# Kernel optimization log

Measured on AMD Instinct MI355X. Metric: run time of the kernel, lower is better.

Reference implementation:

```python
import jax, jax.numpy as jnp
import numpy as np

N_NODES = 20000
N_EDGES = 320000
NUM_GRAPHS = 64
IN_DIM = 256


def setup_inputs() -> dict:
    key = jax.random.key(0)
    ks = jax.random.split(key, 12)
    x = jax.random.normal(ks[0], (N_NODES, IN_DIM), dtype=jnp.float32)
    edge_index = jax.random.randint(ks[1], (2, N_EDGES), 0, N_NODES, dtype=jnp.int64)
    batch = jnp.sort(jax.random.randint(ks[2], (N_NODES,), 0, NUM_GRAPHS, dtype=jnp.int64))
    def glorot(k, shape):
        lim = float(np.sqrt(6.0 / (shape[0] + shape[1])))
        return jax.random.uniform(k, shape, dtype=jnp.float32, minval=-lim, maxval=lim)
    W1 = glorot(ks[3], (IN_DIM, 256)); b1 = jnp.zeros((256,), jnp.float32)
    W2 = glorot(ks[4], (256, 128));   b2 = jnp.zeros((128,), jnp.float32)
    Wl1 = glorot(ks[5], (128, 64));   bl1 = jnp.zeros((64,), jnp.float32)
    Wl2 = glorot(ks[6], (64, 1));     bl2 = jnp.zeros((1,), jnp.float32)
    return {"x": x, "edge_index": edge_index, "batch": batch,
            "W1": W1, "b1": b1, "W2": W2, "b2": b2,
            "Wl1": Wl1, "bl1": bl1, "Wl2": Wl2, "bl2": bl2}


def gcn_conv(x, src, dst, W, b, n_nodes):
    # PyG GCNConv: add self-loops, symmetric normalization D^-1/2 (A+I) D^-1/2,
    # linear transform first, then gather-scale-scatter aggregation, then bias.
    loop = jnp.arange(n_nodes, dtype=src.dtype)
    s = jnp.concatenate([src, loop])
    d = jnp.concatenate([dst, loop])
    deg = jax.ops.segment_sum(jnp.ones_like(d, dtype=x.dtype), d, num_segments=n_nodes)
    dinv = jnp.where(deg > 0, jax.lax.rsqrt(deg), 0.0)
    norm = dinv[s] * dinv[d]                         # [E+N]
    h = x @ W                                        # [N, out]
    msg = h[s] * norm[:, None]                       # [E+N, out]
    out = jax.ops.segment_sum(msg, d, num_segments=n_nodes)
    return out + b


def global_mean_pool(x, batch, num_graphs):
    sums = jax.ops.segment_sum(x, batch, num_segments=num_graphs)
    cnts = jax.ops.segment_sum(jnp.ones((x.shape[0],), x.dtype), batch, num_segments=num_graphs)
    return sums / jnp.maximum(cnts, 1.0)[:, None]


def reference(x, edge_index, batch, W1, b1, W2, b2, Wl1, bl1, Wl2, bl2):
    n = x.shape[0]
    src, dst = edge_index[0], edge_index[1]
    h = jax.nn.relu(gcn_conv(x, src, dst, W1, b1, n))   # dropout = identity (eval)
    h = jax.nn.relu(gcn_conv(h, src, dst, W2, b2, n))
    g = global_mean_pool(h, batch, NUM_GRAPHS)          # [G, 128]
    g = jax.nn.relu(g @ Wl1 + bl1)
    return jax.nn.sigmoid(g @ Wl2 + bl2)                # [G, 1]
```

## Files before the change

### kernel.cpp

```cpp
#include <hip/hip_runtime.h>
#include <hip/hip_bf16.h>
#include <math.h>

typedef __attribute__((ext_vector_type(8))) short bf16x8;
typedef __attribute__((ext_vector_type(4))) float f32x4;

__device__ __forceinline__ unsigned short f2bf(float f) {
    unsigned int u = __float_as_uint(f);
    unsigned int r = (u + 0x7FFFu + ((u >> 16) & 1u)) >> 16;
    return (unsigned short)r;
}
__device__ __forceinline__ unsigned int pk2bf(float lo, float hi) {
    unsigned int r;
    asm("v_cvt_pk_bf16_f32 %0, %1, %2" : "=v"(r) : "v"(lo), "v"(hi));
    return r;
}
__device__ __forceinline__ unsigned char f2fp8(float v) {
    int p = __builtin_amdgcn_cvt_pk_fp8_f32(v, v, 0, false);
    return (unsigned char)(p & 0xff);
}
__device__ __forceinline__ unsigned int pk4fp8(float a, float b, float c, float d) {
    int p = __builtin_amdgcn_cvt_pk_fp8_f32(a, b, 0, false);
    p = __builtin_amdgcn_cvt_pk_fp8_f32(c, d, p, true);
    return (unsigned int)p;
}
__device__ __forceinline__ void fp8x8_fma(uint2 u, float w, float* a) {
    a[0] += __builtin_amdgcn_cvt_f32_fp8((int)u.x, 0) * w;
    a[1] += __builtin_amdgcn_cvt_f32_fp8((int)u.x, 1) * w;
    a[2] += __builtin_amdgcn_cvt_f32_fp8((int)u.x, 2) * w;
    a[3] += __builtin_amdgcn_cvt_f32_fp8((int)u.x, 3) * w;
    a[4] += __builtin_amdgcn_cvt_f32_fp8((int)u.y, 0) * w;
    a[5] += __builtin_amdgcn_cvt_f32_fp8((int)u.y, 1) * w;
    a[6] += __builtin_amdgcn_cvt_f32_fp8((int)u.y, 2) * w;
    a[7] += __builtin_amdgcn_cvt_f32_fp8((int)u.y, 3) * w;
}
__device__ __forceinline__ void fp8x4_fma(unsigned int u, float w, float* a) {
    a[0] += __builtin_amdgcn_cvt_f32_fp8((int)u, 0) * w;
    a[1] += __builtin_amdgcn_cvt_f32_fp8((int)u, 1) * w;
    a[2] += __builtin_amdgcn_cvt_f32_fp8((int)u, 2) * w;
    a[3] += __builtin_amdgcn_cvt_f32_fp8((int)u, 3) * w;
}
__device__ __forceinline__ float deg_dinv(int c) { return rsqrtf((float)c + 1.0f); }

__device__ __forceinline__ void load_lds16(const unsigned short* g, unsigned short* l) {
    __builtin_amdgcn_global_load_lds(
        (const __attribute__((address_space(1))) unsigned int*)g,
        (__attribute__((address_space(3))) unsigned int*)l, 16, 0, 0);
}
__device__ __forceinline__ void load_lds16_u8(const unsigned char* g, unsigned char* l) {
    __builtin_amdgcn_global_load_lds(
        (const __attribute__((address_space(1))) unsigned int*)g,
        (__attribute__((address_space(3))) unsigned int*)l, 16, 0, 0);
}

__global__ __launch_bounds__(256) void prep_kernel(const int* __restrict__ batch,
                                                   int* __restrict__ gstart,
                                                   const float* __restrict__ W1,
                                                   unsigned short* __restrict__ w1t,
                                                   const float* __restrict__ W2,
                                                   unsigned char* __restrict__ w2t8,
                                                   int N, int G, int BNB) {
    int b = blockIdx.x;
    int tid = threadIdx.x;
    if (b < BNB) {
        int i = b * 256 + tid;
        if (i >= N) return;
        int bb = batch[i];
        if (i == 0) { for (int g = 0; g <= bb; g++) gstart[g] = 0; }
        else { int bp = batch[i - 1]; for (int g = bp + 1; g <= bb; g++) gstart[g] = i; }
        if (i == N - 1) { for (int g = bb + 1; g <= G; g++) gstart[g] = N; }
        return;
    }
    int idx = (b - BNB) * 256 + tid;
    if (idx < 256 * 256) {
        int m = idx >> 8, k = idx & 255;
        w1t[idx] = f2bf(W1[(size_t)k * 256 + m]);
    } else if (idx < 256 * 256 + 128 * 256) {
        int j = idx - 256 * 256;
        int m = j >> 8, k = j & 255;
        w2t8[j] = f2fp8(W2[(size_t)k * 128 + m]);
    }
}

__global__ __launch_bounds__(256) void fill_gemm1_kernel(const int* __restrict__ src,
                                                         const int* __restrict__ dst,
                                                         int* __restrict__ cnt,
                                                         int* __restrict__ csr,
                                                         const float* __restrict__ x,
                                                         const unsigned short* __restrict__ Bt,
                                                         unsigned char* __restrict__ C8,
                                                         int N, int E, int FB) {
    __shared__ unsigned short As[128 * 32];
    __shared__ unsigned short Bs[128 * 32];
    if ((int)blockIdx.x < FB) {
        int e = (blockIdx.x * 256 + threadIdx.x) * 4;
        if (e + 3 < E) {
            int4 d4 = *(const int4*)(dst + e);
            int4 s4 = *(const int4*)(src + e);
            int sl;
            sl = atomicAdd(&cnt[d4.x], 1); if (sl < 64) csr[(d4.x << 6) + sl] = s4.x;
            sl = atomicAdd(&cnt[d4.y], 1); if (sl < 64) csr[(d4.y << 6) + sl] = s4.y;
            sl = atomicAdd(&cnt[d4.z], 1); if (sl < 64) csr[(d4.z << 6) + sl] = s4.z;
            sl = atomicAdd(&cnt[d4.w], 1); if (sl < 64) csr[(d4.w << 6) + sl] = s4.w;
        } else {
            for (; e < E; e++) {
                int d = dst[e];
                int slot = atomicAdd(&cnt[d], 1);
                if (slot < 64) csr[(d << 6) + slot] = src[e];
            }
        }
        return;
    }
    int gb = blockIdx.x - FB;
    int bx = gb & 1, by = gb >> 1;
    const int K = 256;
    int tid = threadIdx.x;
    int wave = tid >> 6, lane = tid & 63;
    int quad = lane >> 4, m16 = lane & 15;
    int r0 = by * 128, c0 = bx * 128;
    int srow = lane >> 2;
    int skoff = (lane & 3) * 8;

    f32x4 acc[2][8];
#pragma unroll
    for (int rg = 0; rg < 2; rg++)
#pragma unroll
        for (int ct = 0; ct < 8; ct++) acc[rg][ct] = (f32x4){0.f, 0.f, 0.f, 0.f};

    int arow = tid >> 1, akh = tid & 1;
    int agrow = r0 + arow; if (agrow >= N) agrow = N - 1;
    const float* ap = x + (size_t)agrow * K + akh * 16;
    int asw = (arow >> 1) & 3;
    unsigned short* as0 = As + arow * 32 + ((((akh << 1) | 0) ^ asw) << 3);
    unsigned short* as1 = As + arow * 32 + ((((akh << 1) | 1) ^ asw) << 3);
    int rsw = (m16 >> 1) & 3;

    for (int kb = 0; kb < K; kb += 32) {
        float4 f0 = *(const float4*)(ap + kb);
        float4 f1 = *(const float4*)(ap + kb + 4);
        float4 f2 = *(const float4*)(ap + kb + 8);
        float4 f3 = *(const float4*)(ap + kb + 12);
        {
            int bcol = wave * 16 + srow;
            load_lds16(Bt + (size_t)(c0 + bcol) * K + kb + skoff, Bs + (wave * 16) * 32);
            load_lds16(Bt + (size_t)(c0 + 64 + bcol) * K + kb + skoff, Bs + (64 + wave * 16) * 32);
        }
        uint4 u0, u1;
        u0.x = pk2bf(f0.x, f0.y); u0.y = pk2bf(f0.z, f0.w);
        u0.z = pk2bf(f1.x, f1.y); u0.w = pk2bf(f1.z, f1.w);
        u1.x = pk2bf(f2.x, f2.y); u1.y = pk2bf(f2.z, f2.w);
        u1.z = pk2bf(f3.x, f3.y); u1.w = pk2bf(f3.z, f3.w);
        *(uint4*)as0 = u0;
        *(uint4*)as1 = u1;
        __syncthreads();
        bf16x8 af[2], bfr[8];
#pragma unroll
        for (int rg = 0; rg < 2; rg++)
            af[rg] = *(const bf16x8*)(As + (wave * 32 + rg * 16 + m16) * 32 + ((quad ^ rsw) << 3));
#pragma unroll
        for (int ct = 0; ct < 8; ct++)
            bfr[ct] = *(const bf16x8*)(Bs + (ct * 16 + m16) * 32 + (quad << 3));
#pragma unroll
        for (int rg = 0; rg < 2; rg++)
#pragma unroll
            for (int ct = 0; ct < 8; ct++)
                acc[rg][ct] = __builtin_amdgcn_mfma_f32_16x16x32_bf16(af[rg], bfr[ct], acc[rg][ct], 0, 0, 0);
        __syncthreads();
    }
#pragma unroll
    for (int rg = 0; rg < 2; rg++) {
#pragma unroll
        for (int ct = 0; ct < 8; ct++) {
            int col = c0 + ct * 16 + m16;
#pragma unroll
            for (int r = 0; r < 4; r++) {
                int row = r0 + wave * 32 + rg * 16 + quad * 4 + r;
                if (row < N) C8[(size_t)row * 256 + col] = f2fp8(acc[rg][ct][r]);
            }
        }
    }
}

__global__ __launch_bounds__(256) void gemm2_kernel(const unsigned char* __restrict__ A,
                                                    const unsigned char* __restrict__ Bt,
                                                    unsigned char* __restrict__ C8, int N) {
    __shared__ unsigned char As8[128 * 32];
    __shared__ unsigned char Bs8[64 * 32];
    const int K = 256;
    int tid = threadIdx.x;
    int wave = tid >> 6, lane = tid & 63;
    int quad = lane >> 4, m16 = lane & 15;
    int bx = blockIdx.x, by = blockIdx.y;
    int r0 = by * 128, c0 = bx * 64;

    f32x4 acc[2][4];
#pragma unroll
    for (int rg = 0; rg < 2; rg++)
#pragma unroll
        for (int ct = 0; ct < 4; ct++) acc[rg][ct] = (f32x4){0.f, 0.f, 0.f, 0.f};

    int arow = wave * 32 + (lane >> 1);
    int agrow = r0 + arow; if (agrow >= N) agrow = N - 1;
    int ach = (lane & 1) * 16;
    int brow = (wave & 1) * 32 + (lane >> 1);
    int bch = (lane & 1) * 16;

    for (int kb = 0; kb < K; kb += 32) {
        load_lds16_u8(A + (size_t)agrow * K + kb + ach, As8 + (wave * 32) * 32);
        if (wave < 2)
            load_lds16_u8(Bt + (size_t)(c0 + brow) * K + kb + bch, Bs8 + (wave * 32) * 32);
        __syncthreads();
        long af[2], bfr[4];
#pragma unroll
        for (int rg = 0; rg < 2; rg++)
            af[rg] = *(const long*)(As8 + (wave * 32 + rg * 16 + m16) * 32 + (quad << 3));
#pragma unroll
        for (int ct = 0; ct < 4; ct++)
            bfr[ct] = *(const long*)(Bs8 + (ct * 16 + m16) * 32 + (quad << 3));
#pragma unroll
        for (int rg = 0; rg < 2; rg++)
#pragma unroll
            for (int ct = 0; ct < 4; ct++)
                acc[rg][ct] = __builtin_amdgcn_mfma_f32_16x16x32_fp8_fp8(af[rg], bfr[ct], acc[rg][ct], 0, 0, 0);
        __syncthreads();
    }
#pragma unroll
    for (int rg = 0; rg < 2; rg++) {
#pragma unroll
        for (int ct = 0; ct < 4; ct++) {
            int col = c0 + ct * 16 + m16;
#pragma unroll
            for (int r = 0; r < 4; r++) {
                int row = r0 + wave * 32 + rg * 16 + quad * 4 + r;
                if (row < N) C8[(size_t)row * 128 + col] = f2fp8(acc[rg][ct][r]);
            }
        }
    }
}

__global__ __launch_bounds__(256) void gather256_kernel(const unsigned char* __restrict__ h8,
                                                        const int* __restrict__ csr,
                                                        const int* __restrict__ cnt,
                                                        const float* __restrict__ bias,
                                                        unsigned char* __restrict__ o18, int N) {
    int node = blockIdx.x * 4 + (threadIdx.x >> 6);
    if (node >= N) return;
    int lane = threadIdx.x & 63;
    int half = lane >> 5, hl = lane & 31;
    int beg = node << 6;
    int c = cnt[node]; if (c > 64) c = 64;
    int end = beg + c;
    float a[8] = {0, 0, 0, 0, 0, 0, 0, 0};
    int j = beg;
    for (; j + 7 < end; j += 8) {
        int s0 = csr[j + half], s1 = csr[j + 2 + half];
        int s2 = csr[j + 4 + half], s3 = csr[j + 6 + half];
        float w0 = deg_dinv(cnt[s0]), w1 = deg_dinv(cnt[s1]);
        float w2 = deg_dinv(cnt[s2]), w3 = deg_dinv(cnt[s3]);
        uint2 u0 = *(const uint2*)(h8 + (size_t)s0 * 256 + hl * 8);
        uint2 u1 = *(const uint2*)(h8 + (size_t)s1 * 256 + hl * 8);
        uint2 u2 = *(const uint2*)(h8 + (size_t)s2 * 256 + hl * 8);
        uint2 u3 = *(const uint2*)(h8 + (size_t)s3 * 256 + hl * 8);
        fp8x8_fma(u0, w0, a); fp8x8_fma(u1, w1, a);
        fp8x8_fma(u2, w2, a); fp8x8_fma(u3, w3, a);
    }
    for (; j + 1 < end; j += 2) {
        int s0 = csr[j + half];
        float w0 = deg_dinv(cnt[s0]);
        uint2 u0 = *(const uint2*)(h8 + (size_t)s0 * 256 + hl * 8);
        fp8x8_fma(u0, w0, a);
    }
    if (j < end && half == 0) {
        int s0 = csr[j];
        float w0 = deg_dinv(cnt[s0]);
        uint2 u0 = *(const uint2*)(h8 + (size_t)s0 * 256 + hl * 8);
        fp8x8_fma(u0, w0, a);
    }
#pragma unroll
    for (int i = 0; i < 8; i++) a[i] += __shfl_down(a[i], 32);
    if (half == 0) {
        float dd = deg_dinv(c);
        float self[8] = {0, 0, 0, 0, 0, 0, 0, 0};
        uint2 uh = *(const uint2*)(h8 + (size_t)node * 256 + hl * 8);
        fp8x8_fma(uh, dd, self);
        float4 bv0 = ((const float4*)bias)[hl * 2];
        float4 bv1 = ((const float4*)bias)[hl * 2 + 1];
        float bvf[8] = {bv0.x, bv0.y, bv0.z, bv0.w, bv1.x, bv1.y, bv1.z, bv1.w};
        float v[8];
#pragma unroll
        for (int i = 0; i < 8; i++) v[i] = fmaxf((a[i] + self[i]) * dd + bvf[i], 0.f);
        uint2 o;
        o.x = pk4fp8(v[0], v[1], v[2], v[3]);
        o.y = pk4fp8(v[4], v[5], v[6], v[7]);
        ((uint2*)(o18 + (size_t)node * 256))[hl] = o;
    }
}

__global__ __launch_bounds__(256) void gather128_kernel(const unsigned char* __restrict__ t8,
                                                        const int* __restrict__ csr,
                                                        const int* __restrict__ cnt,
                                                        const float* __restrict__ bias,
                                                        unsigned char* __restrict__ out2, int N) {
    int node = blockIdx.x * 4 + (threadIdx.x >> 6);
    if (node >= N) return;
    int lane = threadIdx.x & 63;
    int half = lane >> 5, hl = lane & 31;
    int beg = node << 6;
    int c = cnt[node]; if (c > 64) c = 64;
    int end = beg + c;
    float a[4] = {0, 0, 0, 0};
    int j = beg;
    for (; j + 7 < end; j += 8) {
        int s0 = csr[j + half], s1 = csr[j + 2 + half];
        int s2 = csr[j + 4 + half], s3 = csr[j + 6 + half];
        float w0 = deg_dinv(cnt[s0]), w1 = deg_dinv(cnt[s1]);
        float w2 = deg_dinv(cnt[s2]), w3 = deg_dinv(cnt[s3]);
        unsigned int u0 = *(const unsigned int*)(t8 + (size_t)s0 * 128 + hl * 4);
        unsigned int u1 = *(const unsigned int*)(t8 + (size_t)s1 * 128 + hl * 4);
        unsigned int u2 = *(const unsigned int*)(t8 + (size_t)s2 * 128 + hl * 4);
        unsigned int u3 = *(const unsigned int*)(t8 + (size_t)s3 * 128 + hl * 4);
        fp8x4_fma(u0, w0, a); fp8x4_fma(u1, w1, a);
        fp8x4_fma(u2, w2, a); fp8x4_fma(u3, w3, a);
    }
    for (; j + 1 < end; j += 2) {
        int s0 = csr[j + half];
        float w0 = deg_dinv(cnt[s0]);
        unsigned int u0 = *(const unsigned int*)(t8 + (size_t)s0 * 128 + hl * 4);
        fp8x4_fma(u0, w0, a);
    }
    if (j < end && half == 0) {
        int s0 = csr[j];
        float w0 = deg_dinv(cnt[s0]);
        unsigned int u0 = *(const unsigned int*)(t8 + (size_t)s0 * 128 + hl * 4);
        fp8x4_fma(u0, w0, a);
    }
#pragma unroll
    for (int i = 0; i < 4; i++) a[i] += __shfl_down(a[i], 32);
    if (half == 0) {
        float dd = deg_dinv(c);
        float self[4] = {0, 0, 0, 0};
        unsigned int uh = *(const unsigned int*)(t8 + (size_t)node * 128 + hl * 4);
        fp8x4_fma(uh, dd, self);
        float4 bv = ((const float4*)bias)[hl];
        float r0 = fmaxf((a[0] + self[0]) * dd + bv.x, 0.f);
        float r1 = fmaxf((a[1] + self[1]) * dd + bv.y, 0.f);
        float r2 = fmaxf((a[2] + self[2]) * dd + bv.z, 0.f);
        float r3 = fmaxf((a[3] + self[3]) * dd + bv.w, 0.f);
        ((unsigned int*)(out2 + (size_t)node * 128))[hl] = pk4fp8(r0, r1, r2, r3);
    }
}

__global__ __launch_bounds__(256) void poolhead_kernel(const unsigned char* __restrict__ out2,
                                                       const int* __restrict__ gstart,
                                                       float* __restrict__ gsum,
                                                       int* __restrict__ gdone,
                                                       const float* __restrict__ Wl1,
                                                       const float* __restrict__ bl1,
                                                       const float* __restrict__ Wl2,
                                                       const float* __restrict__ bl2,
                                                       float* __restrict__ out) {
    int g = blockIdx.x >> 3, slice = blockIdx.x & 7;
    int tid = threadIdx.x;
    int hw = tid >> 5, hl = tid & 31;
    int gs = gstart[g], ge = gstart[g + 1];
    float a[4] = {0, 0, 0, 0};
    for (int i = gs + slice * 8 + hw; i < ge; i += 64) {
        unsigned int u = ((const unsigned int*)(out2 + (size_t)i * 128))[hl];
        fp8x4_fma(u, 1.0f, a);
    }
    __shared__ float red[8][128];
#pragma unroll
    for (int k = 0; k < 4; k++) red[hw][hl * 4 + k] = a[k];
    __syncthreads();
    if (tid < 128) {
        float s = 0.f;
#pragma unroll
        for (int w = 0; w < 8; w++) s += red[w][tid];
        if (s != 0.f) atomicAdd(&gsum[g * 128 + tid], s);
    }
    __syncthreads();
    __shared__ int lastflag;
    if (tid == 0) {
        __threadfence();
        int old = atomicAdd(&gdone[g], 1);
        lastflag = (old == 7) ? 1 : 0;
    }
    __syncthreads();
    if (!lastflag) return;
    __shared__ float gv[128];
    if (tid < 128) {
        float s = atomicAdd(&gsum[g * 128 + tid], 0.0f);
        float cntf = fmaxf((float)(ge - gs), 1.0f);
        gv[tid] = s / cntf;
    }
    __syncthreads();
    if (tid < 64) {
        float acc = bl1[tid];
#pragma unroll 8
        for (int k = 0; k < 128; k++) acc += gv[k] * Wl1[k * 64 + tid];
        acc = fmaxf(acc, 0.f);
        float p = acc * Wl2[tid];
#pragma unroll
        for (int off = 32; off; off >>= 1) p += __shfl_down(p, off);
        if (tid == 0) out[g] = 1.f / (1.f + expf(-(p + bl2[0])));
    }
}

extern "C" void kernel_launch(void* const* d_in, const int* in_sizes, int n_in,
                              void* d_out, int out_size, void* d_ws, size_t ws_size,
                              hipStream_t stream) {
    const float* x   = (const float*)d_in[0];
    const int* ei    = (const int*)d_in[1];
    const int* batch = (const int*)d_in[2];
    const float* W1  = (const float*)d_in[3];
    const float* b1  = (const float*)d_in[4];
    const float* W2  = (const float*)d_in[5];
    const float* b2  = (const float*)d_in[6];
    const float* Wl1 = (const float*)d_in[7];
    const float* bl1 = (const float*)d_in[8];
    const float* Wl2 = (const float*)d_in[9];
    const float* bl2 = (const float*)d_in[10];
    float* out = (float*)d_out;

    const int N = in_sizes[2];
    const int E = in_sizes[1] / 2;
    const int G = 64;
    const int* src = ei;
    const int* dst = ei + E;

    char* base = (char*)d_ws;
    size_t off = 0;
    auto carve = [&](size_t bytes) -> char* {
        char* p = base + off;
        off = (off + bytes + 15) & ~(size_t)15;
        return p;
    };
    int*   cnt    = (int*)carve((size_t)N * 4);
    float* gsum   = (float*)carve((size_t)G * 128 * 4);
    int*   gdone  = (int*)carve((size_t)G * 4);
    size_t zero_bytes = (size_t)(N + G * 128 + G) * 4 + 32;
    int*   csr    = (int*)carve((size_t)N * 64 * 4);
    int*   gstart = (int*)carve((size_t)(G + 1) * 4);
    unsigned short* w1t  = (unsigned short*)carve((size_t)256 * 256 * 2);
    unsigned char*  w2t8 = (unsigned char*)carve((size_t)128 * 256);
    unsigned char*  h8   = (unsigned char*)carve((size_t)N * 256);
    unsigned char*  o18  = (unsigned char*)carve((size_t)N * 256);
    unsigned char*  t8   = h8;
    unsigned char*  out2 = o18;

    hipMemsetAsync(d_ws, 0, zero_bytes, stream);

    const int BNB = (N + 255) / 256;
    const int CWB = (256 * 256 + 128 * 256 + 255) / 256;
    prep_kernel<<<BNB + CWB, 256, 0, stream>>>(batch, gstart, W1, w1t, W2, w2t8, N, G, BNB);

    const int FB  = (E / 4 + 255) / 256;
    const int GB1 = 2 * ((N + 127) / 128);
    fill_gemm1_kernel<<<FB + GB1, 256, 0, stream>>>(src, dst, cnt, csr,
                                                    x, w1t, h8, N, E, FB);

    gather256_kernel<<<(N + 3) / 4, 256, 0, stream>>>(h8, csr, cnt, b1, o18, N);

    {
        dim3 grid(2, (N + 127) / 128);
        gemm2_kernel<<<grid, 256, 0, stream>>>(o18, w2t8, t8, N);
    }
    gather128_kernel<<<(N + 3) / 4, 256, 0, stream>>>(t8, csr, cnt, b2, out2, N);

    poolhead_kernel<<<G * 8, 256, 0, stream>>>(out2, gstart, gsum, gdone,
                                               Wl1, bl1, Wl2, bl2, out);
}
```

Baseline: 171.2 us.

## Fold source-degree normalization into GEMM epilogues and reorganize kernel fusion

Premultiplies each GEMM output row by its dinv so the gather kernels no longer load cnt[src] and compute rsqrt per edge; gathers become plain fp8 sums. Edge CSR fill is moved into the prep kernel so GEMM1 can read final degrees, which costs fusing fill with GEMM1 concurrency. Gather loops are unrolled to 16 neighbours and use packed fp8->f32 conversion when available. Pre-scaling before fp8 quantization slightly changes rounding behaviour.

After: 173.1 us. Within noise of the previous version (+1.1%).

```diff
diff --git a/kernel.cpp b/kernel.cpp
--- a/kernel.cpp
+++ b/kernel.cpp
@@ -4,6 +4,7 @@
 
 typedef __attribute__((ext_vector_type(8))) short bf16x8;
 typedef __attribute__((ext_vector_type(4))) float f32x4;
+typedef __attribute__((ext_vector_type(2))) float f32x2;
 
 __device__ __forceinline__ unsigned short f2bf(float f) {
     unsigned int u = __float_as_uint(f);
@@ -24,22 +25,38 @@
     p = __builtin_amdgcn_cvt_pk_fp8_f32(c, d, p, true);
     return (unsigned int)p;
 }
-__device__ __forceinline__ void fp8x8_fma(uint2 u, float w, float* a) {
-    a[0] += __builtin_amdgcn_cvt_f32_fp8((int)u.x, 0) * w;
-    a[1] += __builtin_amdgcn_cvt_f32_fp8((int)u.x, 1) * w;
-    a[2] += __builtin_amdgcn_cvt_f32_fp8((int)u.x, 2) * w;
-    a[3] += __builtin_amdgcn_cvt_f32_fp8((int)u.x, 3) * w;
-    a[4] += __builtin_amdgcn_cvt_f32_fp8((int)u.y, 0) * w;
-    a[5] += __builtin_amdgcn_cvt_f32_fp8((int)u.y, 1) * w;
-    a[6] += __builtin_amdgcn_cvt_f32_fp8((int)u.y, 2) * w;
-    a[7] += __builtin_amdgcn_cvt_f32_fp8((int)u.y, 3) * w;
-}
-__device__ __forceinline__ void fp8x4_fma(unsigned int u, float w, float* a) {
-    a[0] += __builtin_amdgcn_cvt_f32_fp8((int)u, 0) * w;
-    a[1] += __builtin_amdgcn_cvt_f32_fp8((int)u, 1) * w;
-    a[2] += __builtin_amdgcn_cvt_f32_fp8((int)u, 2) * w;
-    a[3] += __builtin_amdgcn_cvt_f32_fp8((int)u, 3) * w;
-}
+#if __has_builtin(__builtin_amdgcn_cvt_pk_f32_fp8)
+__device__ __forceinline__ void fp8x8_add(uint2 u, float* a) {
+    f32x2 p0 = __builtin_amdgcn_cvt_pk_f32_fp8((int)u.x, false);
+    f32x2 p1 = __builtin_amdgcn_cvt_pk_f32_fp8((int)u.x, true);
+    f32x2 p2 = __builtin_amdgcn_cvt_pk_f32_fp8((int)u.y, false);
+    f32x2 p3 = __builtin_amdgcn_cvt_pk_f32_fp8((int)u.y, true);
+    a[0] += p0.x; a[1] += p0.y; a[2] += p1.x; a[3] += p1.y;
+    a[4] += p2.x; a[5] += p2.y; a[6] += p3.x; a[7] += p3.y;
+}
+__device__ __forceinline__ void fp8x4_add(unsigned int u, float* a) {
+    f32x2 p0 = __builtin_amdgcn_cvt_pk_f32_fp8((int)u, false);
+    f32x2 p1 = __builtin_amdgcn_cvt_pk_f32_fp8((int)u, true);
+    a[0] += p0.x; a[1] += p0.y; a[2] += p1.x; a[3] += p1.y;
+}
+#else
+__device__ __forceinline__ void fp8x8_add(uint2 u, float* a) {
+    a[0] += __builtin_amdgcn_cvt_f32_fp8((int)u.x, 0);
+    a[1] += __builtin_amdgcn_cvt_f32_fp8((int)u.x, 1);
+    a[2] += __builtin_amdgcn_cvt_f32_fp8((int)u.x, 2);
+    a[3] += __builtin_amdgcn_cvt_f32_fp8((int)u.x, 3);
+    a[4] += __builtin_amdgcn_cvt_f32_fp8((int)u.y, 0);
+    a[5] += __builtin_amdgcn_cvt_f32_fp8((int)u.y, 1);
+    a[6] += __builtin_amdgcn_cvt_f32_fp8((int)u.y, 2);
+    a[7] += __builtin_amdgcn_cvt_f32_fp8((int)u.y, 3);
+}
+__device__ __forceinline__ void fp8x4_add(unsigned int u, float* a) {
+    a[0] += __builtin_amdgcn_cvt_f32_fp8((int)u, 0);
+    a[1] += __builtin_amdgcn_cvt_f32_fp8((int)u, 1);
+    a[2] += __builtin_amdgcn_cvt_f32_fp8((int)u, 2);
+    a[3] += __builtin_amdgcn_cvt_f32_fp8((int)u, 3);
+}
+#endif
 __device__ __forceinline__ float deg_dinv(int c) { return rsqrtf((float)c + 1.0f); }
 
 __device__ __forceinline__ void load_lds16(const unsigned short* g, unsigned short* l) {
@@ -53,47 +70,21 @@
         (__attribute__((address_space(3))) unsigned int*)l, 16, 0, 0);
 }
 
-__global__ __launch_bounds__(256) void prep_kernel(const int* __restrict__ batch,
-                                                   int* __restrict__ gstart,
-                                                   const float* __restrict__ W1,
-                                                   unsigned short* __restrict__ w1t,
-                                                   const float* __restrict__ W2,
-                                                   unsigned char* __restrict__ w2t8,
-                                                   int N, int G, int BNB) {
+__global__ __launch_bounds__(256) void prepfill_kernel(const int* __restrict__ src,
+                                                       const int* __restrict__ dst,
+                                                       int* __restrict__ cnt,
+                                                       int* __restrict__ csr,
+                                                       const int* __restrict__ batch,
+                                                       int* __restrict__ gstart,
+                                                       const float* __restrict__ W1,
+                                                       unsigned short* __restrict__ w1t,
+                                                       const float* __restrict__ W2,
+                                                       unsigned char* __restrict__ w2t8,
+                                                       int N, int G, int E, int FB, int CWB) {
     int b = blockIdx.x;
     int tid = threadIdx.x;
-    if (b < BNB) {
-        int i = b * 256 + tid;
-        if (i >= N) return;
-        int bb = batch[i];
-        if (i == 0) { for (int g = 0; g <= bb; g++) gstart[g] = 0; }
-        else { int bp = batch[i - 1]; for (int g = bp + 1; g <= bb; g++) gstart[g] = i; }
-        if (i == N - 1) { for (int g = bb + 1; g <= G; g++) gstart[g] = N; }
-        return;
-    }
-    int idx = (b - BNB) * 256 + tid;
-    if (idx < 256 * 256) {
-        int m = idx >> 8, k = idx & 255;
-        w1t[idx] = f2bf(W1[(size_t)k * 256 + m]);
-    } else if (idx < 256 * 256 + 128 * 256) {
-        int j = idx - 256 * 256;
-        int m = j >> 8, k = j & 255;
-        w2t8[j] = f2fp8(W2[(size_t)k * 128 + m]);
-    }
-}
-
-__global__ __launch_bounds__(256) void fill_gemm1_kernel(const int* __restrict__ src,
-                                                         const int* __restrict__ dst,
-                                                         int* __restrict__ cnt,
-                                                         int* __restrict__ csr,
-                                                         const float* __restrict__ x,
-                                                         const unsigned short* __restrict__ Bt,
-                                                         unsigned char* __restrict__ C8,
-                                                         int N, int E, int FB) {
-    __shared__ unsigned short As[128 * 32];
-    __shared__ unsigned short Bs[128 * 32];
-    if ((int)blockIdx.x < FB) {
-        int e = (blockIdx.x * 256 + threadIdx.x) * 4;
+    if (b < FB) {
+        int e = (b * 256 + tid) * 4;
         if (e + 3 < E) {
             int4 d4 = *(const int4*)(dst + e);
             int4 s4 = *(const int4*)(src + e);
@@ -111,7 +102,37 @@
         }
         return;
     }
-    int gb = blockIdx.x - FB;
+    b -= FB;
+    if (b < CWB) {
+        int idx = b * 256 + tid;
+        if (idx < 256 * 256) {
+            int m = idx >> 8, k = idx & 255;
+            w1t[idx] = f2bf(W1[(size_t)k * 256 + m]);
+        } else if (idx < 256 * 256 + 128 * 256) {
+            int j = idx - 256 * 256;
+            int m = j >> 8, k = j & 255;
+            w2t8[j] = f2fp8(W2[(size_t)k * 128 + m]);
+        }
+        return;
+    }
+    b -= CWB;
+    {
+        int i = b * 256 + tid;
+        if (i >= N) return;
+        int bb = batch[i];
+        if (i == 0) { for (int g = 0; g <= bb; g++) gstart[g] = 0; }
+        else { int bp = batch[i - 1]; for (int g = bp + 1; g <= bb; g++) gstart[g] = i; }
+        if (i == N - 1) { for (int g = bb + 1; g <= G; g++) gstart[g] = N; }
+    }
+}
+
+__global__ __launch_bounds__(256) void gemm1_kernel(const float* __restrict__ x,
+                                                    const unsigned short* __restrict__ Bt,
+                                                    const int* __restrict__ cnt,
+                                                    unsigned char* __restrict__ C8, int N) {
+    __shared__ unsigned short As[128 * 32];
+    __shared__ unsigned short Bs[128 * 32];
+    int gb = blockIdx.x;
     int bx = gb & 1, by = gb >> 1;
     const int K = 256;
     int tid = threadIdx.x;
@@ -167,6 +188,14 @@
                 acc[rg][ct] = __builtin_amdgcn_mfma_f32_16x16x32_bf16(af[rg], bfr[ct], acc[rg][ct], 0, 0, 0);
         __syncthreads();
     }
+    float di[2][4];
+#pragma unroll
+    for (int rg = 0; rg < 2; rg++)
+#pragma unroll
+        for (int r = 0; r < 4; r++) {
+            int row = r0 + wave * 32 + rg * 16 + quad * 4 + r;
+            di[rg][r] = (row < N) ? deg_dinv(cnt[row]) : 1.f;
+        }
 #pragma unroll
     for (int rg = 0; rg < 2; rg++) {
 #pragma unroll
@@ -175,7 +204,7 @@
 #pragma unroll
             for (int r = 0; r < 4; r++) {
                 int row = r0 + wave * 32 + rg * 16 + quad * 4 + r;
-                if (row < N) C8[(size_t)row * 256 + col] = f2fp8(acc[rg][ct][r]);
+                if (row < N) C8[(size_t)row * 256 + col] = f2fp8(acc[rg][ct][r] * di[rg][r]);
             }
         }
     }
@@ -183,6 +212,7 @@
 
 __global__ __launch_bounds__(256) void gemm2_kernel(const unsigned char* __restrict__ A,
                                                     const unsigned char* __restrict__ Bt,
+                                                    const int* __restrict__ cnt,
                                                     unsigned char* __restrict__ C8, int N) {
     __shared__ unsigned char As8[128 * 32];
     __shared__ unsigned char Bs8[64 * 32];
@@ -224,6 +254,14 @@
                 acc[rg][ct] = __builtin_amdgcn_mfma_f32_16x16x32_fp8_fp8(af[rg], bfr[ct], acc[rg][ct], 0, 0, 0);
         __syncthreads();
     }
+    float di[2][4];
+#pragma unroll
+    for (int rg = 0; rg < 2; rg++)
+#pragma unroll
+        for (int r = 0; r < 4; r++) {
+            int row = r0 + wave * 32 + rg * 16 + quad * 4 + r;
+            di[rg][r] = (row < N) ? deg_dinv(cnt[row]) : 1.f;
+        }
 #pragma unroll
     for (int rg = 0; rg < 2; rg++) {
 #pragma unroll
@@ -232,7 +270,7 @@
 #pragma unroll
             for (int r = 0; r < 4; r++) {
                 int row = r0 + wave * 32 + rg * 16 + quad * 4 + r;
-                if (row < N) C8[(size_t)row * 128 + col] = f2fp8(acc[rg][ct][r]);
+                if (row < N) C8[(size_t)row * 128 + col] = f2fp8(acc[rg][ct][r] * di[rg][r]);
             }
         }
     }
@@ -248,41 +286,53 @@
     int lane = threadIdx.x & 63;
     int half = lane >> 5, hl = lane & 31;
     int beg = node << 6;
-    int c = cnt[node]; if (c > 64) c = 64;
+    int c = cnt[node];
+    float dd = deg_dinv(c);
+    if (c > 64) c = 64;
     int end = beg + c;
+    uint2 uh = *(const uint2*)(h8 + (size_t)node * 256 + hl * 8);
     float a[8] = {0, 0, 0, 0, 0, 0, 0, 0};
     int j = beg;
-    for (; j + 7 < end; j += 8) {
-        int s0 = csr[j + half], s1 = csr[j + 2 + half];
-        int s2 = csr[j + 4 + half], s3 = csr[j + 6 + half];
-        float w0 = deg_dinv(cnt[s0]), w1 = deg_dinv(cnt[s1]);
-        float w2 = deg_dinv(cnt[s2]), w3 = deg_dinv(cnt[s3]);
+    for (; j + 15 < end; j += 16) {
+        int s0 = csr[j + half],      s1 = csr[j + 2 + half];
+        int s2 = csr[j + 4 + half],  s3 = csr[j + 6 + half];
+        int s4 = csr[j + 8 + half],  s5 = csr[j + 10 + half];
+        int s6 = csr[j + 12 + half], s7 = csr[j + 14 + half];
         uint2 u0 = *(const uint2*)(h8 + (size_t)s0 * 256 + hl * 8);
         uint2 u1 = *(const uint2*)(h8 + (size_t)s1 * 256 + hl * 8);
         uint2 u2 = *(const uint2*)(h8 + (size_t)s2 * 256 + hl * 8);
         uint2 u3 = *(const uint2*)(h8 + (size_t)s3 * 256 + hl * 8);
-        fp8x8_fma(u0, w0, a); fp8x8_fma(u1, w1, a);
-        fp8x8_fma(u2, w2, a); fp8x8_fma(u3, w3, a);
+        uint2 u4 = *(const uint2*)(h8 + (size_t)s4 * 256 + hl * 8);
+        uint2 u5 = *(const uint2*)(h8 + (size_t)s5 * 256 + hl * 8);
+        uint2 u6 = *(const uint2*)(h8 + (size_t)s6 * 256 + hl * 8);
+        uint2 u7 = *(const uint2*)(h8 + (size_t)s7 * 256 + hl * 8);
+        fp8x8_add(u0, a); fp8x8_add(u1, a); fp8x8_add(u2, a); fp8x8_add(u3, a);
+        fp8x8_add(u4, a); fp8x8_add(u5, a); fp8x8_add(u6, a); fp8x8_add(u7, a);
+    }
+    for (; j + 7 < end; j += 8) {
+        int s0 = csr[j + half], s1 = csr[j + 2 + half];
+        int s2 = csr[j + 4 + half], s3 = csr[j + 6 + half];
+        uint2 u0 = *(const uint2*)(h8 + (size_t)s0 * 256 + hl * 8);
+        uint2 u1 = *(const uint2*)(h8 + (size_t)s1 * 256 + hl * 8);
+        uint2 u2 = *(const uint2*)(h8 + (size_t)s2 * 256 + hl * 8);
+        uint2 u3 = *(const uint2*)(h8 + (size_t)s3 * 256 + hl * 8);
+        fp8x8_add(u0, a); fp8x8_add(u1, a); fp8x8_add(u2, a); fp8x8_add(u3, a);
     }
     for (; j + 1 < end; j += 2) {
         int s0 = csr[j + half];
-        float w0 = deg_dinv(cnt[s0]);
         uint2 u0 = *(const uint2*)(h8 + (size_t)s0 * 256 + hl * 8);
-        fp8x8_fma(u0, w0, a);
+        fp8x8_add(u0, a);
     }
     if (j < end && half == 0) {
         int s0 = csr[j];
-        float w0 = deg_dinv(cnt[s0]);
         uint2 u0 = *(const uint2*)(h8 + (size_t)s0 * 256 + hl * 8);
-        fp8x8_fma(u0, w0, a);
+        fp8x8_add(u0, a);
     }
 #pragma unroll
     for (int i = 0; i < 8; i++) a[i] += __shfl_down(a[i], 32);
     if (half == 0) {
-        float dd = deg_dinv(c);
         float self[8] = {0, 0, 0, 0, 0, 0, 0, 0};
-        uint2 uh = *(const uint2*)(h8 + (size_t)node * 256 + hl * 8);
-        fp8x8_fma(uh, dd, self);
+        fp8x8_add(uh, self);
         float4 bv0 = ((const float4*)bias)[hl * 2];
         float4 bv1 = ((const float4*)bias)[hl * 2 + 1];
         float bvf[8] = {bv0.x, bv0.y, bv0.z, bv0.w, bv1.x, bv1.y, bv1.z, bv1.w};
@@ -306,41 +356,53 @@
     int lane = threadIdx.x & 63;
     int half = lane >> 5, hl = lane & 31;
     int beg = node << 6;
-    int c = cnt[node]; if (c > 64) c = 64;
+    int c = cnt[node];
+    float dd = deg_dinv(c);
+    if (c > 64) c = 64;
     int end = beg + c;
+    unsigned int uh = *(const unsigned int*)(t8 + (size_t)node * 128 + hl * 4);
     float a[4] = {0, 0, 0, 0};
     int j = beg;
-    for (; j + 7 < end; j += 8) {
-        int s0 = csr[j + half], s1 = csr[j + 2 + half];
-        int s2 = csr[j + 4 + half], s3 = csr[j + 6 + half];
-        float w0 = deg_dinv(cnt[s0]), w1 = deg_dinv(cnt[s1]);
-        float w2 = deg_dinv(cnt[s2]), w3 = deg_dinv(cnt[s3]);
+    for (; j + 15 < end; j += 16) {
+        int s0 = csr[j + half],      s1 = csr[j + 2 + half];
+        int s2 = csr[j + 4 + half],  s3 = csr[j + 6 + half];
+        int s4 = csr[j + 8 + half],  s5 = csr[j + 10 + half];
+        int s6 = csr[j + 12 + half], s7 = csr[j + 14 + half];
         unsigned int u0 = *(const unsigned int*)(t8 + (size_t)s0 * 128 + hl * 4);
         unsigned int u1 = *(const unsigned int*)(t8 + (size_t)s1 * 128 + hl * 4);
         unsigned int u2 = *(const unsigned int*)(t8 + (size_t)s2 * 128 + hl * 4);
         unsigned int u3 = *(const unsigned int*)(t8 + (size_t)s3 * 128 + hl * 4);
-        fp8x4_fma(u0, w0, a); fp8x4_fma(u1, w1, a);
-        fp8x4_fma(u2, w2, a); fp8x4_fma(u3, w3, a);
+        unsigned int u4 = *(const unsigned int*)(t8 + (size_t)s4 * 128 + hl * 4);
+        unsigned int u5 = *(const unsigned int*)(t8 + (size_t)s5 * 128 + hl * 4);
+        unsigned int u6 = *(const unsigned int*)(t8 + (size_t)s6 * 128 + hl * 4);
+        unsigned int u7 = *(const unsigned int*)(t8 + (size_t)s7 * 128 + hl * 4);
+        fp8x4_add(u0, a); fp8x4_add(u1, a); fp8x4_add(u2, a); fp8x4_add(u3, a);
+        fp8x4_add(u4, a); fp8x4_add(u5, a); fp8x4_add(u6, a); fp8x4_add(u7, a);
+    }
+    for (; j + 7 < end; j += 8) {
+        int s0 = csr[j + half], s1 = csr[j + 2 + half];
+        int s2 = csr[j + 4 + half], s3 = csr[j + 6 + half];
+        unsigned int u0 = *(const unsigned int*)(t8 + (size_t)s0 * 128 + hl * 4);
+        unsigned int u1 = *(const unsigned int*)(t8 + (size_t)s1 * 128 + hl * 4);
+        unsigned int u2 = *(const unsigned int*)(t8 + (size_t)s2 * 128 + hl * 4);
+        unsigned int u3 = *(const unsigned int*)(t8 + (size_t)s3 * 128 + hl * 4);
+        fp8x4_add(u0, a); fp8x4_add(u1, a); fp8x4_add(u2, a); fp8x4_add(u3, a);
     }
     for (; j + 1 < end; j += 2) {
         int s0 = csr[j + half];
-        float w0 = deg_dinv(cnt[s0]);
         unsigned int u0 = *(const unsigned int*)(t8 + (size_t)s0 * 128 + hl * 4);
-        fp8x4_fma(u0, w0, a);
+        fp8x4_add(u0, a);
     }
     if (j < end && half == 0) {
         int s0 = csr[j];
-        float w0 = deg_dinv(cnt[s0]);
         unsigned int u0 = *(const unsigned int*)(t8 + (size_t)s0 * 128 + hl * 4);
-        fp8x4_fma(u0, w0, a);
+        fp8x4_add(u0, a);
     }
 #pragma unroll
     for (int i = 0; i < 4; i++) a[i] += __shfl_down(a[i], 32);
     if (half == 0) {
-        float dd = deg_dinv(c);
         float self[4] = {0, 0, 0, 0};
-        unsigned int uh = *(const unsigned int*)(t8 + (size_t)node * 128 + hl * 4);
-        fp8x4_fma(uh, dd, self);
+        fp8x4_add(uh, self);
         float4 bv = ((const float4*)bias)[hl];
         float r0 = fmaxf((a[0] + self[0]) * dd + bv.x, 0.f);
         float r1 = fmaxf((a[1] + self[1]) * dd + bv.y, 0.f);
@@ -366,7 +428,7 @@
     float a[4] = {0, 0, 0, 0};
     for (int i = gs + slice * 8 + hw; i < ge; i += 64) {
         unsigned int u = ((const unsigned int*)(out2 + (size_t)i * 128))[hl];
-        fp8x4_fma(u, 1.0f, a);
+        fp8x4_add(u, a);
     }
     __shared__ float red[8][128];
 #pragma unroll
@@ -452,18 +514,18 @@
 
     const int BNB = (N + 255) / 256;
     const int CWB = (256 * 256 + 128 * 256 + 255) / 256;
-    prep_kernel<<<BNB + CWB, 256, 0, stream>>>(batch, gstart, W1, w1t, W2, w2t8, N, G, BNB);
-
     const int FB  = (E / 4 + 255) / 256;
+    prepfill_kernel<<<FB + CWB + BNB, 256, 0, stream>>>(src, dst, cnt, csr, batch, gstart,
+                                                        W1, w1t, W2, w2t8, N, G, E, FB, CWB);
+
     const int GB1 = 2 * ((N + 127) / 128);
-    fill_gemm1_kernel<<<FB + GB1, 256, 0, stream>>>(src, dst, cnt, csr,
-                                                    x, w1t, h8, N, E, FB);
+    gemm1_kernel<<<GB1, 256, 0, stream>>>(x, w1t, cnt, h8, N);
 
     gather256_kernel<<<(N + 3) / 4, 256, 0, stream>>>(h8, csr, cnt, b1, o18, N);
 
     {
         dim3 grid(2, (N + 127) / 128);
-        gemm2_kernel<<<grid, 256, 0, stream>>>(o18, w2t8, t8, N);
+        gemm2_kernel<<<grid, 256, 0, stream>>>(o18, w2t8, cnt, t8, N);
     }
     gather128_kernel<<<(N + 3) / 4, 256, 0, stream>>>(t8, csr, cnt, b2, out2, N);
 
```
